# Kernel tuning notes

Measured on AMD Instinct MI355X. Metric: run time of the kernel, lower is better.

The kernel has to match this reference:

```python
import jax, jax.numpy as jnp
import numpy as np

N = 50000      # nodes
E = 800000     # edges (before self-loops)
F_IN = 128
H = 4          # heads
C = 64         # per-head channels
G = 64         # graphs in batch
NEG_SLOPE = 0.2


def setup_inputs() -> dict:
    key = jax.random.key(0)
    ks = jax.random.split(key, 20)
    rn = lambda k, shape, s=0.1: (jax.random.normal(k, shape, jnp.float32) * s)
    x = jax.random.normal(ks[0], (N, F_IN), jnp.float32)
    edge_index = jax.random.randint(ks[1], (2, E), 0, N, dtype=jnp.int32)
    batch = jnp.sort(jax.random.randint(ks[2], (N,), 0, G, dtype=jnp.int32))
    return {
        "x": x, "edge_index": edge_index, "batch": batch,
        # layer 0: 128 -> (4 heads x 64), concat
        "W0": rn(ks[3], (F_IN, H * C)), "a_src0": rn(ks[4], (H, C)), "a_dst0": rn(ks[5], (H, C)), "b0": jnp.zeros((H * C,), jnp.float32),
        "W1": rn(ks[6], (H * C, H * C)), "a_src1": rn(ks[7], (H, C)), "a_dst1": rn(ks[8], (H, C)), "b1": jnp.zeros((H * C,), jnp.float32),
        "W2": rn(ks[9], (H * C, C)), "a_src2": rn(ks[10], (1, C)), "a_dst2": rn(ks[11], (1, C)), "b2": jnp.zeros((C,), jnp.float32),
        "lin_w": rn(ks[12], (C, 1)), "lin_b": jnp.zeros((1,), jnp.float32),
    }


def gat_layer(h_in, src, dst, W, a_src, a_dst, b, heads, ch, concat):
    n = h_in.shape[0]
    h = (h_in @ W).reshape(n, heads, ch)                         # [N,H,C]
    e_src = jnp.sum(h * a_src[None], axis=-1)                    # [N,H]
    e_dst = jnp.sum(h * a_dst[None], axis=-1)                    # [N,H]
    e = jax.nn.leaky_relu(e_src[src] + e_dst[dst], NEG_SLOPE)    # [E,H]
    # segment softmax over incoming edges of each destination node
    m = jax.ops.segment_max(e, dst, num_segments=n)
    m = jnp.where(jnp.isneginf(m), 0.0, m)
    ex = jnp.exp(e - m[dst])
    denom = jax.ops.segment_sum(ex, dst, num_segments=n)
    alpha = ex / (denom[dst] + 1e-16)                            # [E,H]
    out = jax.ops.segment_sum(h[src] * alpha[:, :, None], dst, num_segments=n)  # [N,H,C]
    out = out.reshape(n, heads * ch) if concat else out.mean(axis=1)
    return out + b


def reference(x, edge_index, batch, W0, a_src0, a_dst0, b0, W1, a_src1, a_dst1, b1, W2, a_src2, a_dst2, b2, lin_w, lin_b):
    n = x.shape[0]
    loops = jnp.arange(n, dtype=edge_index.dtype)
    src = jnp.concatenate([edge_index[0], loops])  # PyG add_self_loops=True
    dst = jnp.concatenate([edge_index[1], loops])
    h = jax.nn.relu(gat_layer(x, src, dst, W0, a_src0, a_dst0, b0, H, C, True))
    h = jax.nn.relu(gat_layer(h, src, dst, W1, a_src1, a_dst1, b1, H, C, True))
    h = gat_layer(h, src, dst, W2, a_src2, a_dst2, b2, 1, C, False)  # [N,64]
    # global mean pool per graph
    counts = jax.ops.segment_sum(jnp.ones((n,), h.dtype), batch, num_segments=G)
    pooled = jax.ops.segment_sum(h, batch, num_segments=G) / jnp.maximum(counts, 1.0)[:, None]
    return pooled @ lin_w + lin_b  # [G,1]
```

## Files before the change

kernel.cpp:

```cpp
#include <hip/hip_runtime.h>
#include <math.h>

typedef __bf16 bf16x8 __attribute__((ext_vector_type(8)));
typedef __bf16 bf16x4 __attribute__((ext_vector_type(4)));
typedef float f32x4 __attribute__((ext_vector_type(4)));
typedef float f32x2 __attribute__((ext_vector_type(2)));
typedef unsigned int u32x2 __attribute__((ext_vector_type(2)));
typedef unsigned int u32x4 __attribute__((ext_vector_type(4)));

#define LOG2E 1.4426950408889634f
#define BCAP 8192

static __device__ __forceinline__ float lrelu(float e) { return fmaxf(e, 0.2f * e); }
static __device__ __forceinline__ float fexp2(float x) { return __builtin_amdgcn_exp2f(x); }

static __device__ __forceinline__ int cmap(int p) {
  return (p & ~63) + (p & 3) * 16 + ((p & 63) >> 2);
}

__global__ void prep_kernel(const float* __restrict__ W0, __bf16* __restrict__ Bt0,
                            const float* __restrict__ W1, __bf16* __restrict__ Bt1, int FIN,
                            const float* __restrict__ W2, const float* __restrict__ lin_w,
                            const float* __restrict__ a_src2, const float* __restrict__ a_dst2,
                            const float* __restrict__ b2, float* __restrict__ wt,
                            float* __restrict__ vas, float* __restrict__ vad,
                            float* __restrict__ bc, int* __restrict__ cnt, int n) {
  int b = blockIdx.x;
  if (b < 256) {
    for (int k = threadIdx.x; k < FIN; k += 256) Bt0[b * FIN + k] = (__bf16)W0[k * 256 + b];
    return;
  }
  b -= 256;
  if (b < 256) {
    int k = threadIdx.x;
    Bt1[b * 256 + k] = (__bf16)W1[cmap(k) * 256 + b];
    return;
  }
  b -= 256;
  if (b == 0) {
    int c = threadIdx.x;
    float qv = 0.f, sv = 0.f, dv = 0.f;
    for (int k = 0; k < 64; k++) {
      float wv = W2[c * 64 + k];
      qv += wv * lin_w[k];
      sv += wv * a_src2[k];
      dv += wv * a_dst2[k];
    }
    wt[c] = qv;
    vas[c] = sv;
    vad[c] = dv;
    if (c == 0) {
      float s = 0.f;
      for (int k = 0; k < 64; k++) s += b2[k] * lin_w[k];
      bc[0] = s;
    }
    return;
  }
  b -= 1;
  int i = b * 256 + threadIdx.x;
  if (i < n) cnt[i] = 0;
}

template <int K, int NT>
__global__ __launch_bounds__(256) void gemm_part_kernel(
    const float* __restrict__ A, const __bf16* __restrict__ Bt,
    const float* __restrict__ a_src, const float* __restrict__ a_dst,
    unsigned char* __restrict__ C, float* __restrict__ es, float* __restrict__ ed, int M,
    int gmx, const int* __restrict__ srcE, const int* __restrict__ dstE,
    int* __restrict__ bucket_cnt, unsigned int* __restrict__ part, int E, int EE, int n) {
  constexpr int Nc = NT * 64;
  constexpr int H = NT;
  constexpr int KS = K / 32;
  __shared__ __bf16 Bs[2][NT * 64][40];
  if ((int)blockIdx.x >= gmx) {
    int tid = threadIdx.x;
    int* hist = (int*)&Bs[0][0][0];
    int* gbase = hist + 256;
    hist[tid] = 0;
    __syncthreads();
    int ab = ((int)blockIdx.x - gmx) * 4096;
    int sv[16], dv[16];
#pragma unroll
    for (int t = 0; t < 16; t++) {
      int e = ab + t * 256 + tid;
      if (e < EE) {
        if (e < E) { sv[t] = srcE[e]; dv[t] = dstE[e]; }
        else { sv[t] = dv[t] = e - E; }
      } else { sv[t] = -1; dv[t] = 0; }
    }
    int lr[16];
#pragma unroll
    for (int t = 0; t < 16; t++)
      if (sv[t] >= 0) lr[t] = atomicAdd(&hist[dv[t] >> 8], 1);
    __syncthreads();
    int NB = (n + 255) >> 8;
    gbase[tid] = (tid < NB && hist[tid] > 0) ? atomicAdd(&bucket_cnt[tid * 16], hist[tid]) : 0;
    __syncthreads();
#pragma unroll
    for (int t = 0; t < 16; t++)
      if (sv[t] >= 0) {
        int bk = dv[t] >> 8;
        part[(size_t)bk * BCAP + gbase[bk] + lr[t]] =
            (unsigned int)sv[t] | ((unsigned int)(dv[t] & 255) << 24);
      }
    return;
  }
  int bid = blockIdx.x;
  int tid = threadIdx.x;
  int wave = tid >> 6;
  int lane = tid & 63;
  int quad = lane >> 4;
  int l16 = lane & 15;
  int rowBase = bid * 64 + wave * 16;
  f32x4 acc[NT * 4] = {};
  int arow = rowBase + l16;
  arow = (arow < M) ? arow : (M - 1);
  const float* Aptr = &A[(size_t)arow * K + quad * 8];
  int sr = tid >> 2;
  int sc = (tid & 3) * 8;
  bf16x8 af[KS];
#pragma unroll
  for (int s = 0; s < KS; s++) {
    f32x4 lo = *(const f32x4*)&Aptr[s * 32];
    f32x4 hi = *(const f32x4*)&Aptr[s * 32 + 4];
    bf16x8 t;
    t[0] = (__bf16)lo.x; t[1] = (__bf16)lo.y; t[2] = (__bf16)lo.z; t[3] = (__bf16)lo.w;
    t[4] = (__bf16)hi.x; t[5] = (__bf16)hi.y; t[6] = (__bf16)hi.z; t[7] = (__bf16)hi.w;
    af[s] = t;
  }
#pragma unroll
  for (int it = 0; it < NT; it++) {
    int r = it * 64 + sr;
    *(bf16x8*)&Bs[0][r][sc] = *(const bf16x8*)&Bt[(size_t)r * K + sc];
  }
  __syncthreads();
#pragma unroll
  for (int s = 0; s < KS; s++) {
    int cur = s & 1;
    if (s + 1 < KS) {
#pragma unroll
      for (int it = 0; it < NT; it++) {
        int r = it * 64 + sr;
        *(bf16x8*)&Bs[cur ^ 1][r][sc] = *(const bf16x8*)&Bt[(size_t)r * K + (s + 1) * 32 + sc];
      }
    }
#pragma unroll
    for (int ng = 0; ng < NT * 4; ng++) {
      bf16x8 b = *(const bf16x8*)&Bs[cur][ng * 16 + l16][quad * 8];
      acc[ng] = __builtin_amdgcn_mfma_f32_16x16x32_bf16(af[s], b, acc[ng], 0, 0, 0);
    }
    __syncthreads();
  }
  float asv[NT * 4], adv[NT * 4];
#pragma unroll
  for (int ng = 0; ng < NT * 4; ng++) {
    int c = (ng >> 2) * 64 + (ng & 3) * 16 + l16;
    asv[ng] = a_src[c];
    adv[ng] = a_dst[c];
  }
#pragma unroll
  for (int r = 0; r < 4; r++) {
    int row = rowBase + quad * 4 + r;
#pragma unroll
    for (int h = 0; h < H; h++) {
      float ss = 0.f, sd = 0.f;
#pragma unroll
      for (int g = 0; g < 4; g++) {
        float hv = acc[h * 4 + g][r];
        ss += hv * asv[h * 4 + g];
        sd += hv * adv[h * 4 + g];
      }
#pragma unroll
      for (int o = 1; o < 16; o <<= 1) {
        ss += __shfl_xor(ss, o);
        sd += __shfl_xor(sd, o);
      }
      if (row < M) {
        if (l16 == 0) {
          es[row * H + h] = ss * LOG2E;
          ed[row * H + h] = sd * LOG2E;
        }
        unsigned int pk = 0;
        pk = __builtin_amdgcn_cvt_pk_fp8_f32(acc[h * 4 + 0][r], acc[h * 4 + 1][r], pk, false);
        pk = __builtin_amdgcn_cvt_pk_fp8_f32(acc[h * 4 + 2][r], acc[h * 4 + 3][r], pk, true);
        *(unsigned int*)&C[(size_t)row * Nc + h * 64 + l16 * 4] = pk;
      }
    }
  }
}

__global__ __launch_bounds__(1024) void bucket_csr_kernel(
    const unsigned int* __restrict__ part, const int* __restrict__ bucket_cnt,
    int* __restrict__ offsets, int* __restrict__ src_sorted, int n, int EE) {
  __shared__ int sc[256];
  __shared__ int excl[256];
  __shared__ int run[256];
  int tid = threadIdx.x;
  int b = blockIdx.x;
  int NB = (n + 255) >> 8;
  if (tid < 256) sc[tid] = (tid < NB) ? bucket_cnt[tid * 16] : 0;
  __syncthreads();
  for (int d = 1; d < 256; d <<= 1) {
    int t = 0;
    if (tid < 256 && tid >= d) t = sc[tid - d];
    __syncthreads();
    if (tid < 256) sc[tid] += t;
    __syncthreads();
  }
  int base = (b == 0) ? 0 : sc[b - 1];
  int cb = sc[b] - base;
  const unsigned int* mypart = part + (size_t)b * BCAP;
  if (tid < 256) run[tid] = 0;
  __syncthreads();
  for (int i = tid; i < cb; i += 1024) atomicAdd(&run[mypart[i] >> 24], 1);
  __syncthreads();
  int myc = (tid < 256) ? run[tid] : 0;
  if (tid < 256) sc[tid] = myc;
  __syncthreads();
  for (int d = 1; d < 256; d <<= 1) {
    int t = 0;
    if (tid < 256 && tid >= d) t = sc[tid - d];
    __syncthreads();
    if (tid < 256) sc[tid] += t;
    __syncthreads();
  }
  if (tid < 256) {
    excl[tid] = sc[tid] - myc;
    int node = b * 256 + tid;
    if (node < n) offsets[node] = base + excl[tid];
    run[tid] = 0;
  }
  if (b == 0 && tid == 0) offsets[n] = EE;
  __syncthreads();
  for (int i = tid; i < cb; i += 1024) {
    unsigned int p = mypart[i];
    int j = p >> 24;
    int r = atomicAdd(&run[j], 1);
    src_sorted[base + excl[j] + r] = (int)(p & 0xFFFFFFu);
  }
}

template <int K, int NT>
__global__ __launch_bounds__(256) void gemm2_kernel(const __bf16* __restrict__ A,
                                                    const __bf16* __restrict__ Bt,
                                                    const float* __restrict__ a_src,
                                                    const float* __restrict__ a_dst,
                                                    unsigned char* __restrict__ C,
                                                    float* __restrict__ es,
                                                    float* __restrict__ ed, int M) {
  constexpr int Nc = NT * 64;
  constexpr int H = NT;
  constexpr int KS = K / 32;
  __shared__ __bf16 Bs[2][NT * 64][40];
  int tid = threadIdx.x;
  int wave = tid >> 6;
  int lane = tid & 63;
  int quad = lane >> 4;
  int l16 = lane & 15;
  int rowBase = blockIdx.x * 64 + wave * 16;
  f32x4 acc[NT * 4] = {};
  int arow = rowBase + l16;
  arow = (arow < M) ? arow : (M - 1);
  const __bf16* Aptr = &A[(size_t)arow * K + quad * 8];
  int sr = tid >> 2;
  int sc = (tid & 3) * 8;
  bf16x8 af[KS];
#pragma unroll
  for (int s = 0; s < KS; s++) af[s] = *(const bf16x8*)&Aptr[s * 32];
#pragma unroll
  for (int it = 0; it < NT; it++) {
    int r = it * 64 + sr;
    *(bf16x8*)&Bs[0][r][sc] = *(const bf16x8*)&Bt[(size_t)r * K + sc];
  }
  __syncthreads();
#pragma unroll
  for (int s = 0; s < KS; s++) {
    int cur = s & 1;
    if (s + 1 < KS) {
#pragma unroll
      for (int it = 0; it < NT; it++) {
        int r = it * 64 + sr;
        *(bf16x8*)&Bs[cur ^ 1][r][sc] = *(const bf16x8*)&Bt[(size_t)r * K + (s + 1) * 32 + sc];
      }
    }
#pragma unroll
    for (int ng = 0; ng < NT * 4; ng++) {
      bf16x8 b = *(const bf16x8*)&Bs[cur][ng * 16 + l16][quad * 8];
      acc[ng] = __builtin_amdgcn_mfma_f32_16x16x32_bf16(af[s], b, acc[ng], 0, 0, 0);
    }
    __syncthreads();
  }
  float asv[NT * 4], adv[NT * 4];
#pragma unroll
  for (int ng = 0; ng < NT * 4; ng++) {
    int c = (ng >> 2) * 64 + (ng & 3) * 16 + l16;
    asv[ng] = a_src[c];
    adv[ng] = a_dst[c];
  }
#pragma unroll
  for (int r = 0; r < 4; r++) {
    int row = rowBase + quad * 4 + r;
#pragma unroll
    for (int h = 0; h < H; h++) {
      float ss = 0.f, sd = 0.f;
#pragma unroll
      for (int g = 0; g < 4; g++) {
        float hv = acc[h * 4 + g][r];
        ss += hv * asv[h * 4 + g];
        sd += hv * adv[h * 4 + g];
      }
#pragma unroll
      for (int o = 1; o < 16; o <<= 1) {
        ss += __shfl_xor(ss, o);
        sd += __shfl_xor(sd, o);
      }
      if (row < M) {
        if (l16 == 0) {
          es[row * H + h] = ss * LOG2E;
          ed[row * H + h] = sd * LOG2E;
        }
        unsigned int pk = 0;
        pk = __builtin_amdgcn_cvt_pk_fp8_f32(acc[h * 4 + 0][r], acc[h * 4 + 1][r], pk, false);
        pk = __builtin_amdgcn_cvt_pk_fp8_f32(acc[h * 4 + 2][r], acc[h * 4 + 3][r], pk, true);
        *(unsigned int*)&C[(size_t)row * Nc + h * 64 + l16 * 4] = pk;
      }
    }
  }
}

__global__ void agg256_kernel(const unsigned char* __restrict__ h, const int* __restrict__ offsets,
                              const int* __restrict__ src_sorted, const float* __restrict__ es,
                              const float* __restrict__ ed, const float* __restrict__ bias,
                              __bf16* __restrict__ out, int n) {
  int node = blockIdx.x * (blockDim.x >> 6) + (threadIdx.x >> 6);
  int lane = threadIdx.x & 63;
  if (node >= n) return;
  int quad = lane >> 4;
  int l16 = lane & 15;
  unsigned hd = (unsigned)(l16 >> 2);
  unsigned cOff = (unsigned)(l16 * 16);
  float myEd = ed[node * 4 + hd];
  int off = offsets[node];
  int deg = offsets[node + 1] - off;
  int idxr = (lane < deg) ? src_sorted[off + lane] : 0;
  float acc[16] = {};
  float sw = 0.f;
  int npre = (deg < 64 ? deg : 64) & ~7;
  int j = 0;
  float eA0 = 0.f, eA1 = 0.f;
  u32x4 uA0 = {}, uA1 = {};
  if (j + 8 <= npre) {
    unsigned sA0 = (unsigned)__shfl(idxr, j + quad);
    unsigned sA1 = (unsigned)__shfl(idxr, j + 4 + quad);
    eA0 = es[sA0 * 4u + hd];
    eA1 = es[sA1 * 4u + hd];
    uA0 = *(const u32x4*)(h + (sA0 << 8) + cOff);
    uA1 = *(const u32x4*)(h + (sA1 << 8) + cOff);
  }
  while (j + 8 <= npre) {
    int jn = j + 8;
    float eB0 = 0.f, eB1 = 0.f;
    u32x4 uB0 = {}, uB1 = {};
    if (jn + 8 <= npre) {
      unsigned sB0 = (unsigned)__shfl(idxr, jn + quad);
      unsigned sB1 = (unsigned)__shfl(idxr, jn + 4 + quad);
      eB0 = es[sB0 * 4u + hd];
      eB1 = es[sB1 * 4u + hd];
      uB0 = *(const u32x4*)(h + (sB0 << 8) + cOff);
      uB1 = *(const u32x4*)(h + (sB1 << 8) + cOff);
    }
    float w0 = fexp2(lrelu(eA0 + myEd));
    float w1 = fexp2(lrelu(eA1 + myEd));
    sw += w0 + w1;
#pragma unroll
    for (int i = 0; i < 4; i++) {
      f32x2 a = __builtin_amdgcn_cvt_pk_f32_fp8(uA0[i], false);
      f32x2 b = __builtin_amdgcn_cvt_pk_f32_fp8(uA0[i], true);
      acc[i * 4 + 0] += w0 * a.x;
      acc[i * 4 + 1] += w0 * a.y;
      acc[i * 4 + 2] += w0 * b.x;
      acc[i * 4 + 3] += w0 * b.y;
    }
#pragma unroll
    for (int i = 0; i < 4; i++) {
      f32x2 a = __builtin_amdgcn_cvt_pk_f32_fp8(uA1[i], false);
      f32x2 b = __builtin_amdgcn_cvt_pk_f32_fp8(uA1[i], true);
      acc[i * 4 + 0] += w1 * a.x;
      acc[i * 4 + 1] += w1 * a.y;
      acc[i * 4 + 2] += w1 * b.x;
      acc[i * 4 + 3] += w1 * b.y;
    }
    eA0 = eB0; eA1 = eB1; uA0 = uB0; uA1 = uB1;
    j = jn;
  }
  for (; j < deg; j += 4) {
    if (quad < deg - j) {
      unsigned s = (unsigned)src_sorted[off + j + quad];
      float w = fexp2(lrelu(es[s * 4u + hd] + myEd));
      sw += w;
      u32x4 u = *(const u32x4*)(h + (s << 8) + cOff);
#pragma unroll
      for (int i = 0; i < 4; i++) {
        f32x2 a = __builtin_amdgcn_cvt_pk_f32_fp8(u[i], false);
        f32x2 b = __builtin_amdgcn_cvt_pk_f32_fp8(u[i], true);
        acc[i * 4 + 0] += w * a.x;
        acc[i * 4 + 1] += w * a.y;
        acc[i * 4 + 2] += w * b.x;
        acc[i * 4 + 3] += w * b.y;
      }
    }
  }
  sw += __shfl_xor(sw, 16);
  sw += __shfl_xor(sw, 32);
#pragma unroll
  for (int k = 0; k < 16; k++) {
    acc[k] += __shfl_xor(acc[k], 16);
    acc[k] += __shfl_xor(acc[k], 32);
  }
  float invS = 1.0f / (sw + 1e-16f);
  if (quad == 0) {
    bf16x8 o0, o1;
#pragma unroll
    for (int k = 0; k < 16; k++) {
      int c = (int)hd * 64 + (k & 3) * 16 + (l16 & 3) * 4 + (k >> 2);
      float v = fmaxf(acc[k] * invS + bias[c], 0.f);
      if (k < 8) o0[k] = (__bf16)v; else o1[k - 8] = (__bf16)v;
    }
    *(bf16x8*)&out[(size_t)node * 256 + l16 * 16] = o0;
    *(bf16x8*)&out[(size_t)node * 256 + l16 * 16 + 8] = o1;
  }
}

__global__ void agg256f_kernel(const unsigned char* __restrict__ h, const int* __restrict__ offsets,
                               const int* __restrict__ src_sorted, const float* __restrict__ es,
                               const float* __restrict__ ed, const float* __restrict__ bias,
                               const float* __restrict__ wt, const float* __restrict__ vas,
                               const float* __restrict__ vad, f32x2* __restrict__ qes,
                               float* __restrict__ ed2, int n) {
  int node = blockIdx.x * (blockDim.x >> 6) + (threadIdx.x >> 6);
  int lane = threadIdx.x & 63;
  if (node >= n) return;
  int quad = lane >> 4;
  int l16 = lane & 15;
  unsigned hd = (unsigned)(l16 >> 2);
  unsigned cOff = (unsigned)(l16 * 16);
  float myEd = ed[node * 4 + hd];
  int off = offsets[node];
  int deg = offsets[node + 1] - off;
  int idxr = (lane < deg) ? src_sorted[off + lane] : 0;
  float acc[16] = {};
  float sw = 0.f;
  int npre = (deg < 64 ? deg : 64) & ~7;
  int j = 0;
  float eA0 = 0.f, eA1 = 0.f;
  u32x4 uA0 = {}, uA1 = {};
  if (j + 8 <= npre) {
    unsigned sA0 = (unsigned)__shfl(idxr, j + quad);
    unsigned sA1 = (unsigned)__shfl(idxr, j + 4 + quad);
    eA0 = es[sA0 * 4u + hd];
    eA1 = es[sA1 * 4u + hd];
    uA0 = *(const u32x4*)(h + (sA0 << 8) + cOff);
    uA1 = *(const u32x4*)(h + (sA1 << 8) + cOff);
  }
  while (j + 8 <= npre) {
    int jn = j + 8;
    float eB0 = 0.f, eB1 = 0.f;
    u32x4 uB0 = {}, uB1 = {};
    if (jn + 8 <= npre) {
      unsigned sB0 = (unsigned)__shfl(idxr, jn + quad);
      unsigned sB1 = (unsigned)__shfl(idxr, jn + 4 + quad);
      eB0 = es[sB0 * 4u + hd];
      eB1 = es[sB1 * 4u + hd];
      uB0 = *(const u32x4*)(h + (sB0 << 8) + cOff);
      uB1 = *(const u32x4*)(h + (sB1 << 8) + cOff);
    }
    float w0 = fexp2(lrelu(eA0 + myEd));
    float w1 = fexp2(lrelu(eA1 + myEd));
    sw += w0 + w1;
#pragma unroll
    for (int i = 0; i < 4; i++) {
      f32x2 a = __builtin_amdgcn_cvt_pk_f32_fp8(uA0[i], false);
      f32x2 b = __builtin_amdgcn_cvt_pk_f32_fp8(uA0[i], true);
      acc[i * 4 + 0] += w0 * a.x;
      acc[i * 4 + 1] += w0 * a.y;
      acc[i * 4 + 2] += w0 * b.x;
      acc[i * 4 + 3] += w0 * b.y;
    }
#pragma unroll
    for (int i = 0; i < 4; i++) {
      f32x2 a = __builtin_amdgcn_cvt_pk_f32_fp8(uA1[i], false);
      f32x2 b = __builtin_amdgcn_cvt_pk_f32_fp8(uA1[i], true);
      acc[i * 4 + 0] += w1 * a.x;
      acc[i * 4 + 1] += w1 * a.y;
      acc[i * 4 + 2] += w1 * b.x;
      acc[i * 4 + 3] += w1 * b.y;
    }
    eA0 = eB0; eA1 = eB1; uA0 = uB0; uA1 = uB1;
    j = jn;
  }
  for (; j < deg; j += 4) {
    if (quad < deg - j) {
      unsigned s = (unsigned)src_sorted[off + j + quad];
      float w = fexp2(lrelu(es[s * 4u + hd] + myEd));
      sw += w;
      u32x4 u = *(const u32x4*)(h + (s << 8) + cOff);
#pragma unroll
      for (int i = 0; i < 4; i++) {
        f32x2 a = __builtin_amdgcn_cvt_pk_f32_fp8(u[i], false);
        f32x2 b = __builtin_amdgcn_cvt_pk_f32_fp8(u[i], true);
        acc[i * 4 + 0] += w * a.x;
        acc[i * 4 + 1] += w * a.y;
        acc[i * 4 + 2] += w * b.x;
        acc[i * 4 + 3] += w * b.y;
      }
    }
  }
  sw += __shfl_xor(sw, 16);
  sw += __shfl_xor(sw, 32);
#pragma unroll
  for (int k = 0; k < 16; k++) {
    acc[k] += __shfl_xor(acc[k], 16);
    acc[k] += __shfl_xor(acc[k], 32);
  }
  float invS = 1.0f / (sw + 1e-16f);
  float q = 0.f, s2 = 0.f, d2 = 0.f;
#pragma unroll
  for (int k = 0; k < 16; k++) {
    int c = (int)hd * 64 + (k & 3) * 16 + (l16 & 3) * 4 + (k >> 2);
    float v = fmaxf(acc[k] * invS + bias[c], 0.f);
    q += v * wt[c];
    s2 += v * vas[c];
    d2 += v * vad[c];
  }
#pragma unroll
  for (int o = 1; o < 16; o <<= 1) {
    q += __shfl_xor(q, o);
    s2 += __shfl_xor(s2, o);
    d2 += __shfl_xor(d2, o);
  }
  if (lane == 0) {
    f32x2 r;
    r.x = q;
    r.y = s2 * LOG2E;
    qes[node] = r;
    ed2[node] = d2 * LOG2E;
  }
}

__global__ void agg64v2_kernel(const f32x2* __restrict__ qes, const float* __restrict__ ed2,
                               const int* __restrict__ offsets, const int* __restrict__ src_sorted,
                               const float* __restrict__ bc, float* __restrict__ pnode, int n) {
  int node = blockIdx.x * (blockDim.x >> 6) + (threadIdx.x >> 6);
  int lane = threadIdx.x & 63;
  if (node >= n) return;
  float myEd = ed2[node];
  int off = offsets[node];
  int deg = offsets[node + 1] - off;
  float sw = 0.f, swq = 0.f;
  for (int j = lane; j < deg; j += 64) {
    int s = src_sorted[off + j];
    f32x2 v = qes[s];
    float w = fexp2(lrelu(v.y + myEd));
    sw += w;
    swq += w * v.x;
  }
#pragma unroll
  for (int o = 1; o < 64; o <<= 1) {
    sw += __shfl_xor(sw, o);
    swq += __shfl_xor(swq, o);
  }
  if (lane == 0) pnode[node] = swq / (sw + 1e-16f) + bc[0];
}

static __device__ __forceinline__ int lowerb(const int* __restrict__ a, int n, int key) {
  int lo = 0, hi = n;
  while (lo < hi) {
    int mid = (lo + hi) >> 1;
    if (a[mid] < key) lo = mid + 1; else hi = mid;
  }
  return lo;
}

__global__ void poolfinal_kernel(const float* __restrict__ pnode, const int* __restrict__ batch,
                                 const float* __restrict__ lin_b, float* __restrict__ out, int n) {
  __shared__ float ws[4];
  int g = blockIdx.x;
  int start = lowerb(batch, n, g);
  int end = lowerb(batch, n, g + 1);
  float acc = 0.f;
  for (int i = start + threadIdx.x; i < end; i += 256) acc += pnode[i];
  for (int o = 32; o > 0; o >>= 1) acc += __shfl_down(acc, o);
  if ((threadIdx.x & 63) == 0) ws[threadIdx.x >> 6] = acc;
  __syncthreads();
  if (threadIdx.x == 0) {
    float total = ws[0] + ws[1] + ws[2] + ws[3];
    out[g] = total / fmaxf((float)(end - start), 1.0f) + lin_b[0];
  }
}

extern "C" void kernel_launch(void* const* d_in, const int* in_sizes, int n_in, void* d_out,
                              int out_size, void* d_ws, size_t ws_size, hipStream_t stream) {
  const float* x = (const float*)d_in[0];
  const int* edge_index = (const int*)d_in[1];
  const int* batch = (const int*)d_in[2];
  const float* W0 = (const float*)d_in[3];
  const float* a_src0 = (const float*)d_in[4];
  const float* a_dst0 = (const float*)d_in[5];
  const float* b0 = (const float*)d_in[6];
  const float* W1 = (const float*)d_in[7];
  const float* a_src1 = (const float*)d_in[8];
  const float* a_dst1 = (const float*)d_in[9];
  const float* b1 = (const float*)d_in[10];
  const float* W2 = (const float*)d_in[11];
  const float* a_src2 = (const float*)d_in[12];
  const float* a_dst2 = (const float*)d_in[13];
  const float* b2 = (const float*)d_in[14];
  const float* lin_w = (const float*)d_in[15];
  const float* lin_b = (const float*)d_in[16];
  float* out = (float*)d_out;

  const int N = in_sizes[2];
  const int E = in_sizes[1] / 2;
  const int EE = E + N;
  const int G = 64;
  const int FIN = in_sizes[0] / N;

  const int* srcArr = edge_index;
  const int* dstArr = edge_index + E;

  size_t off = 0;
  auto alloc = [&](size_t bytes) -> void* {
    off = (off + 255) & ~(size_t)255;
    void* p = (char*)d_ws + off;
    off += bytes;
    return p;
  };
  unsigned char* hA = (unsigned char*)alloc((size_t)N * 256);
  __bf16* hB = (__bf16*)alloc((size_t)N * 256 * 2);
  float* pnode = (float*)alloc((size_t)N * 4);
  __bf16* Bt0 = (__bf16*)alloc((size_t)256 * FIN * 2);
  __bf16* Bt1 = (__bf16*)alloc((size_t)256 * 256 * 2);
  float* es = (float*)alloc((size_t)N * 4 * 4);
  float* ed = (float*)alloc((size_t)N * 4 * 4);
  int* offsets = (int*)alloc((size_t)(N + 1) * 4);
  int* src_sorted = (int*)alloc((size_t)EE * 4);
  int* bucket_cnt = (int*)alloc((size_t)4096 * 4);
  f32x2* qes = (f32x2*)alloc((size_t)N * 8);
  float* ed2 = (float*)alloc((size_t)N * 4);
  float* wt = (float*)alloc(256 * 4);
  float* vas = (float*)alloc(256 * 4);
  float* vad = (float*)alloc(256 * 4);
  float* bc = (float*)alloc(256);
  (void)ws_size;

  int NB = (N + 255) >> 8;

  unsigned int* part = (unsigned int*)hB;

  int nwb = (N + 3) / 4;
  int gmx = (N + 63) / 64;
  int nA = (EE + 4095) / 4096;

  prep_kernel<<<256 + 256 + 1 + 16, 256, 0, stream>>>(W0, Bt0, W1, Bt1, FIN, W2, lin_w, a_src2,
                                                      a_dst2, b2, wt, vas, vad, bc, bucket_cnt,
                                                      4096);

  gemm_part_kernel<128, 4><<<gmx + nA, 256, 0, stream>>>(
      x, Bt0, a_src0, a_dst0, hA, es, ed, N, gmx, srcArr, dstArr, bucket_cnt, part, E, EE, N);

  bucket_csr_kernel<<<NB, 1024, 0, stream>>>(part, bucket_cnt, offsets, src_sorted, N, EE);

  agg256_kernel<<<nwb, 256, 0, stream>>>(hA, offsets, src_sorted, es, ed, b0, hB, N);

  gemm2_kernel<256, 4><<<gmx, 256, 0, stream>>>(hB, Bt1, a_src1, a_dst1, hA, es, ed, N);

  agg256f_kernel<<<nwb, 256, 0, stream>>>(hA, offsets, src_sorted, es, ed, b1, wt, vas, vad, qes,
                                          ed2, N);

  agg64v2_kernel<<<nwb, 256, 0, stream>>>(qes, ed2, offsets, src_sorted, bc, pnode, N);

  poolfinal_kernel<<<G, 256, 0, stream>>>(pnode, batch, lin_b, out, N);
}
```

Baseline: 263.4 us.

## Assign one 16-lane group per node in 256-channel aggregation kernels

The two 256-channel aggregation kernels now process one destination node per 16-lane group instead of one per 64-lane wavefront. Each group walks that node's edges serially, two at a time with prefetch. This removes the cross-quad shuffle reductions and the idle lanes on low-degree nodes (about 17 incoming edges on average). In exchange each group has fewer loads in flight per node and a longer serial loop, and high-degree nodes (over 32 edges) fall to a slower scalar tail loop.

```diff
diff --git a/kernel.cpp b/kernel.cpp
--- a/kernel.cpp
+++ b/kernel.cpp
@@ -328,107 +328,90 @@
   }
 }
 
+
+static __device__ __forceinline__ void accum16(const u32x4& u, float w, float* acc) {
+#pragma unroll
+  for (int i = 0; i < 4; i++) {
+    f32x2 a = __builtin_amdgcn_cvt_pk_f32_fp8(u[i], false);
+    f32x2 b = __builtin_amdgcn_cvt_pk_f32_fp8(u[i], true);
+    acc[i * 4 + 0] += w * a.x;
+    acc[i * 4 + 1] += w * a.y;
+    acc[i * 4 + 2] += w * b.x;
+    acc[i * 4 + 3] += w * b.y;
+  }
+}
+
 __global__ void agg256_kernel(const unsigned char* __restrict__ h, const int* __restrict__ offsets,
                               const int* __restrict__ src_sorted, const float* __restrict__ es,
                               const float* __restrict__ ed, const float* __restrict__ bias,
                               __bf16* __restrict__ out, int n) {
-  int node = blockIdx.x * (blockDim.x >> 6) + (threadIdx.x >> 6);
-  int lane = threadIdx.x & 63;
+  int tid = threadIdx.x;
+  int node = blockIdx.x * 16 + (tid >> 4);
   if (node >= n) return;
-  int quad = lane >> 4;
-  int l16 = lane & 15;
-  unsigned hd = (unsigned)(l16 >> 2);
-  unsigned cOff = (unsigned)(l16 * 16);
+  int g16 = tid & 15;
+  int lbase = (tid & 63) & 48;
+  unsigned hd = (unsigned)(g16 >> 2);
+  unsigned cOff = (unsigned)(g16 * 16);
   float myEd = ed[node * 4 + hd];
   int off = offsets[node];
   int deg = offsets[node + 1] - off;
-  int idxr = (lane < deg) ? src_sorted[off + lane] : 0;
+  int idx0 = (g16 < deg) ? src_sorted[off + g16] : 0;
+  int idx1 = (16 + g16 < deg) ? src_sorted[off + 16 + g16] : 0;
+  int nmain = deg < 32 ? deg : 32;
   float acc[16] = {};
   float sw = 0.f;
-  int npre = (deg < 64 ? deg : 64) & ~7;
-  int j = 0;
+  int e = 0;
   float eA0 = 0.f, eA1 = 0.f;
   u32x4 uA0 = {}, uA1 = {};
-  if (j + 8 <= npre) {
-    unsigned sA0 = (unsigned)__shfl(idxr, j + quad);
-    unsigned sA1 = (unsigned)__shfl(idxr, j + 4 + quad);
-    eA0 = es[sA0 * 4u + hd];
-    eA1 = es[sA1 * 4u + hd];
-    uA0 = *(const u32x4*)(h + (sA0 << 8) + cOff);
-    uA1 = *(const u32x4*)(h + (sA1 << 8) + cOff);
-  }
-  while (j + 8 <= npre) {
-    int jn = j + 8;
+  if (e < nmain) {
+    unsigned s = (unsigned)__shfl(e < 16 ? idx0 : idx1, lbase | (e & 15));
+    eA0 = es[s * 4u + hd];
+    uA0 = *(const u32x4*)(h + (s << 8) + cOff);
+  }
+  if (e + 1 < nmain) {
+    unsigned s = (unsigned)__shfl(e + 1 < 16 ? idx0 : idx1, lbase | ((e + 1) & 15));
+    eA1 = es[s * 4u + hd];
+    uA1 = *(const u32x4*)(h + (s << 8) + cOff);
+  }
+  while (e < nmain) {
+    int en = e + 2;
     float eB0 = 0.f, eB1 = 0.f;
     u32x4 uB0 = {}, uB1 = {};
-    if (jn + 8 <= npre) {
-      unsigned sB0 = (unsigned)__shfl(idxr, jn + quad);
-      unsigned sB1 = (unsigned)__shfl(idxr, jn + 4 + quad);
-      eB0 = es[sB0 * 4u + hd];
-      eB1 = es[sB1 * 4u + hd];
-      uB0 = *(const u32x4*)(h + (sB0 << 8) + cOff);
-      uB1 = *(const u32x4*)(h + (sB1 << 8) + cOff);
+    if (en < nmain) {
+      unsigned s = (unsigned)__shfl(en < 16 ? idx0 : idx1, lbase | (en & 15));
+      eB0 = es[s * 4u + hd];
+      uB0 = *(const u32x4*)(h + (s << 8) + cOff);
+    }
+    if (en + 1 < nmain) {
+      unsigned s = (unsigned)__shfl(en + 1 < 16 ? idx0 : idx1, lbase | ((en + 1) & 15));
+      eB1 = es[s * 4u + hd];
+      uB1 = *(const u32x4*)(h + (s << 8) + cOff);
     }
     float w0 = fexp2(lrelu(eA0 + myEd));
-    float w1 = fexp2(lrelu(eA1 + myEd));
+    float w1 = (e + 1 < nmain) ? fexp2(lrelu(eA1 + myEd)) : 0.f;
     sw += w0 + w1;
-#pragma unroll
-    for (int i = 0; i < 4; i++) {
-      f32x2 a = __builtin_amdgcn_cvt_pk_f32_fp8(uA0[i], false);
-      f32x2 b = __builtin_amdgcn_cvt_pk_f32_fp8(uA0[i], true);
-      acc[i * 4 + 0] += w0 * a.x;
-      acc[i * 4 + 1] += w0 * a.y;
-      acc[i * 4 + 2] += w0 * b.x;
-      acc[i * 4 + 3] += w0 * b.y;
-    }
-#pragma unroll
-    for (int i = 0; i < 4; i++) {
-      f32x2 a = __builtin_amdgcn_cvt_pk_f32_fp8(uA1[i], false);
-      f32x2 b = __builtin_amdgcn_cvt_pk_f32_fp8(uA1[i], true);
-      acc[i * 4 + 0] += w1 * a.x;
-      acc[i * 4 + 1] += w1 * a.y;
-      acc[i * 4 + 2] += w1 * b.x;
-      acc[i * 4 + 3] += w1 * b.y;
-    }
+    accum16(uA0, w0, acc);
+    accum16(uA1, w1, acc);
     eA0 = eB0; eA1 = eB1; uA0 = uB0; uA1 = uB1;
-    j = jn;
-  }
-  for (; j < deg; j += 4) {
-    if (quad < deg - j) {
-      unsigned s = (unsigned)src_sorted[off + j + quad];
-      float w = fexp2(lrelu(es[s * 4u + hd] + myEd));
-      sw += w;
-      u32x4 u = *(const u32x4*)(h + (s << 8) + cOff);
-#pragma unroll
-      for (int i = 0; i < 4; i++) {
-        f32x2 a = __builtin_amdgcn_cvt_pk_f32_fp8(u[i], false);
-        f32x2 b = __builtin_amdgcn_cvt_pk_f32_fp8(u[i], true);
-        acc[i * 4 + 0] += w * a.x;
-        acc[i * 4 + 1] += w * a.y;
-        acc[i * 4 + 2] += w * b.x;
-        acc[i * 4 + 3] += w * b.y;
-      }
-    }
-  }
-  sw += __shfl_xor(sw, 16);
-  sw += __shfl_xor(sw, 32);
+    e = en;
+  }
+  for (int t = 32; t < deg; t++) {
+    unsigned s = (unsigned)src_sorted[off + t];
+    float w = fexp2(lrelu(es[s * 4u + hd] + myEd));
+    sw += w;
+    u32x4 u = *(const u32x4*)(h + (s << 8) + cOff);
+    accum16(u, w, acc);
+  }
+  float invS = 1.0f / (sw + 1e-16f);
+  bf16x8 o0, o1;
 #pragma unroll
   for (int k = 0; k < 16; k++) {
-    acc[k] += __shfl_xor(acc[k], 16);
-    acc[k] += __shfl_xor(acc[k], 32);
-  }
-  float invS = 1.0f / (sw + 1e-16f);
-  if (quad == 0) {
-    bf16x8 o0, o1;
-#pragma unroll
-    for (int k = 0; k < 16; k++) {
-      int c = (int)hd * 64 + (k & 3) * 16 + (l16 & 3) * 4 + (k >> 2);
-      float v = fmaxf(acc[k] * invS + bias[c], 0.f);
-      if (k < 8) o0[k] = (__bf16)v; else o1[k - 8] = (__bf16)v;
-    }
-    *(bf16x8*)&out[(size_t)node * 256 + l16 * 16] = o0;
-    *(bf16x8*)&out[(size_t)node * 256 + l16 * 16 + 8] = o1;
-  }
+    int c = (int)hd * 64 + (k & 3) * 16 + (g16 & 3) * 4 + (k >> 2);
+    float v = fmaxf(acc[k] * invS + bias[c], 0.f);
+    if (k < 8) o0[k] = (__bf16)v; else o1[k - 8] = (__bf16)v;
+  }
+  *(bf16x8*)&out[(size_t)node * 256 + g16 * 16] = o0;
+  *(bf16x8*)&out[(size_t)node * 256 + g16 * 16 + 8] = o1;
 }
 
 __global__ void agg256f_kernel(const unsigned char* __restrict__ h, const int* __restrict__ offsets,
@@ -437,96 +420,68 @@
                                const float* __restrict__ wt, const float* __restrict__ vas,
                                const float* __restrict__ vad, f32x2* __restrict__ qes,
                                float* __restrict__ ed2, int n) {
-  int node = blockIdx.x * (blockDim.x >> 6) + (threadIdx.x >> 6);
-  int lane = threadIdx.x & 63;
+  int tid = threadIdx.x;
+  int node = blockIdx.x * 16 + (tid >> 4);
   if (node >= n) return;
-  int quad = lane >> 4;
-  int l16 = lane & 15;
-  unsigned hd = (unsigned)(l16 >> 2);
-  unsigned cOff = (unsigned)(l16 * 16);
+  int g16 = tid & 15;
+  int lbase = (tid & 63) & 48;
+  unsigned hd = (unsigned)(g16 >> 2);
+  unsigned cOff = (unsigned)(g16 * 16);
   float myEd = ed[node * 4 + hd];
   int off = offsets[node];
   int deg = offsets[node + 1] - off;
-  int idxr = (lane < deg) ? src_sorted[off + lane] : 0;
+  int idx0 = (g16 < deg) ? src_sorted[off + g16] : 0;
+  int idx1 = (16 + g16 < deg) ? src_sorted[off + 16 + g16] : 0;
+  int nmain = deg < 32 ? deg : 32;
   float acc[16] = {};
   float sw = 0.f;
-  int npre = (deg < 64 ? deg : 64) & ~7;
-  int j = 0;
+  int e = 0;
   float eA0 = 0.f, eA1 = 0.f;
   u32x4 uA0 = {}, uA1 = {};
-  if (j + 8 <= npre) {
-    unsigned sA0 = (unsigned)__shfl(idxr, j + quad);
-    unsigned sA1 = (unsigned)__shfl(idxr, j + 4 + quad);
-    eA0 = es[sA0 * 4u + hd];
-    eA1 = es[sA1 * 4u + hd];
-    uA0 = *(const u32x4*)(h + (sA0 << 8) + cOff);
-    uA1 = *(const u32x4*)(h + (sA1 << 8) + cOff);
-  }
-  while (j + 8 <= npre) {
-    int jn = j + 8;
+  if (e < nmain) {
+    unsigned s = (unsigned)__shfl(e < 16 ? idx0 : idx1, lbase | (e & 15));
+    eA0 = es[s * 4u + hd];
+    uA0 = *(const u32x4*)(h + (s << 8) + cOff);
+  }
+  if (e + 1 < nmain) {
+    unsigned s = (unsigned)__shfl(e + 1 < 16 ? idx0 : idx1, lbase | ((e + 1) & 15));
+    eA1 = es[s * 4u + hd];
+    uA1 = *(const u32x4*)(h + (s << 8) + cOff);
+  }
+  while (e < nmain) {
+    int en = e + 2;
     float eB0 = 0.f, eB1 = 0.f;
     u32x4 uB0 = {}, uB1 = {};
-    if (jn + 8 <= npre) {
-      unsigned sB0 = (unsigned)__shfl(idxr, jn + quad);
-      unsigned sB1 = (unsigned)__shfl(idxr, jn + 4 + quad);
-      eB0 = es[sB0 * 4u + hd];
-      eB1 = es[sB1 * 4u + hd];
-      uB0 = *(const u32x4*)(h + (sB0 << 8) + cOff);
-      uB1 = *(const u32x4*)(h + (sB1 << 8) + cOff);
+    if (en < nmain) {
+      unsigned s = (unsigned)__shfl(en < 16 ? idx0 : idx1, lbase | (en & 15));
+      eB0 = es[s * 4u + hd];
+      uB0 = *(const u32x4*)(h + (s << 8) + cOff);
+    }
+    if (en + 1 < nmain) {
+      unsigned s = (unsigned)__shfl(en + 1 < 16 ? idx0 : idx1, lbase | ((en + 1) & 15));
+      eB1 = es[s * 4u + hd];
+      uB1 = *(const u32x4*)(h + (s << 8) + cOff);
     }
     float w0 = fexp2(lrelu(eA0 + myEd));
-    float w1 = fexp2(lrelu(eA1 + myEd));
+    float w1 = (e + 1 < nmain) ? fexp2(lrelu(eA1 + myEd)) : 0.f;
     sw += w0 + w1;
-#pragma unroll
-    for (int i = 0; i < 4; i++) {
-      f32x2 a = __builtin_amdgcn_cvt_pk_f32_fp8(uA0[i], false);
-      f32x2 b = __builtin_amdgcn_cvt_pk_f32_fp8(uA0[i], true);
-      acc[i * 4 + 0] += w0 * a.x;
-      acc[i * 4 + 1] += w0 * a.y;
-      acc[i * 4 + 2] += w0 * b.x;
-      acc[i * 4 + 3] += w0 * b.y;
-    }
-#pragma unroll
-    for (int i = 0; i < 4; i++) {
-      f32x2 a = __builtin_amdgcn_cvt_pk_f32_fp8(uA1[i], false);
-      f32x2 b = __builtin_amdgcn_cvt_pk_f32_fp8(uA1[i], true);
-      acc[i * 4 + 0] += w1 * a.x;
-      acc[i * 4 + 1] += w1 * a.y;
-      acc[i * 4 + 2] += w1 * b.x;
-      acc[i * 4 + 3] += w1 * b.y;
-    }
+    accum16(uA0, w0, acc);
+    accum16(uA1, w1, acc);
     eA0 = eB0; eA1 = eB1; uA0 = uB0; uA1 = uB1;
-    j = jn;
-  }
-  for (; j < deg; j += 4) {
-    if (quad < deg - j) {
-      unsigned s = (unsigned)src_sorted[off + j + quad];
-      float w = fexp2(lrelu(es[s * 4u + hd] + myEd));
-      sw += w;
-      u32x4 u = *(const u32x4*)(h + (s << 8) + cOff);
-#pragma unroll
-      for (int i = 0; i < 4; i++) {
-        f32x2 a = __builtin_amdgcn_cvt_pk_f32_fp8(u[i], false);
-        f32x2 b = __builtin_amdgcn_cvt_pk_f32_fp8(u[i], true);
-        acc[i * 4 + 0] += w * a.x;
-        acc[i * 4 + 1] += w * a.y;
-        acc[i * 4 + 2] += w * b.x;
-        acc[i * 4 + 3] += w * b.y;
-      }
-    }
-  }
-  sw += __shfl_xor(sw, 16);
-  sw += __shfl_xor(sw, 32);
-#pragma unroll
-  for (int k = 0; k < 16; k++) {
-    acc[k] += __shfl_xor(acc[k], 16);
-    acc[k] += __shfl_xor(acc[k], 32);
+    e = en;
+  }
+  for (int t = 32; t < deg; t++) {
+    unsigned s = (unsigned)src_sorted[off + t];
+    float w = fexp2(lrelu(es[s * 4u + hd] + myEd));
+    sw += w;
+    u32x4 u = *(const u32x4*)(h + (s << 8) + cOff);
+    accum16(u, w, acc);
   }
   float invS = 1.0f / (sw + 1e-16f);
   float q = 0.f, s2 = 0.f, d2 = 0.f;
 #pragma unroll
   for (int k = 0; k < 16; k++) {
-    int c = (int)hd * 64 + (k & 3) * 16 + (l16 & 3) * 4 + (k >> 2);
+    int c = (int)hd * 64 + (k & 3) * 16 + (g16 & 3) * 4 + (k >> 2);
     float v = fmaxf(acc[k] * invS + bias[c], 0.f);
     q += v * wt[c];
     s2 += v * vas[c];
@@ -538,7 +493,7 @@
     s2 += __shfl_xor(s2, o);
     d2 += __shfl_xor(d2, o);
   }
-  if (lane == 0) {
+  if (g16 == 0) {
     f32x2 r;
     r.x = q;
     r.y = s2 * LOG2E;
@@ -658,6 +613,7 @@
   unsigned int* part = (unsigned int*)hB;
 
   int nwb = (N + 3) / 4;
+  int ngb = (N + 15) / 16;
   int gmx = (N + 63) / 64;
   int nA = (EE + 4095) / 4096;
 
@@ -670,11 +626,11 @@
 
   bucket_csr_kernel<<<NB, 1024, 0, stream>>>(part, bucket_cnt, offsets, src_sorted, N, EE);
 
-  agg256_kernel<<<nwb, 256, 0, stream>>>(hA, offsets, src_sorted, es, ed, b0, hB, N);
+  agg256_kernel<<<ngb, 256, 0, stream>>>(hA, offsets, src_sorted, es, ed, b0, hB, N);
 
   gemm2_kernel<256, 4><<<gmx, 256, 0, stream>>>(hB, Bt1, a_src1, a_dst1, hA, es, ed, N);
 
-  agg256f_kernel<<<nwb, 256, 0, stream>>>(hA, offsets, src_sorted, es, ed, b1, wt, vas, vad, qes,
+  agg256f_kernel<<<ngb, 256, 0, stream>>>(hA, offsets, src_sorted, es, ed, b1, wt, vas, vad, qes,
                                           ed2, N);
 
   agg64v2_kernel<<<nwb, 256, 0, stream>>>(qes, ed2, offsets, src_sorted, bc, pnode, N);
```

New measurement: 272.8 us. 3.6% more time.
